# Kernel tuning notes

Measured on AMD Instinct MI355X. Metric: run time of the kernel, lower is better.

The kernel has to match this reference:

```python
import jax, jax.numpy as jnp
import numpy as np

N_NODES = 200000
N_EDGES = 240000
HIDDEN = 128
N_TYPES = 6


def setup_inputs() -> dict:
    key = jax.random.key(0)
    k1, k2, k3, k4, k5 = jax.random.split(key, 5)
    state_embedding = jax.random.normal(k1, (N_NODES, HIDDEN), dtype=jnp.float32)
    # row 0: edge type in [1, N_TYPES]; row 1: source node; row 2: target node
    etype = jax.random.randint(k2, (N_EDGES,), 1, N_TYPES + 1, dtype=jnp.int32)
    src = jax.random.randint(k3, (N_EDGES,), 0, N_NODES, dtype=jnp.int32)
    tgt = jax.random.randint(k4, (N_EDGES,), 0, N_NODES, dtype=jnp.int32)
    typed_edges = jnp.stack([etype, src, tgt], axis=0)  # [3, E]
    # stacked per-edge-type Linear(2H, H, bias=False) weights, applied as x @ W[t]
    W = jax.random.normal(k5, (N_TYPES, 2 * HIDDEN, HIDDEN), dtype=jnp.float32) / np.sqrt(2 * HIDDEN)
    return {"state_embedding": state_embedding, "typed_edges": typed_edges, "W": W}


def reference(state_embedding, typed_edges, W):
    etype, src, tgt = typed_edges[0], typed_edges[1], typed_edges[2]
    # gather source/target node states and concat -> [E, 2H]
    x = jnp.concatenate([state_embedding[src], state_embedding[tgt]], axis=1)
    n_types = W.shape[0]
    msgs = jnp.zeros((x.shape[0], W.shape[2]), dtype=x.dtype)
    # fixed small loop over edge types; masking replaces the dynamic boolean
    # filtering of the torch code (edges with type t use only W[t-1])
    for t in range(n_types):
        mask = (etype == t + 1)[:, None]
        msgs = msgs + jnp.where(mask, x @ W[t], jnp.zeros((), x.dtype))
    # scatter-add messages into target node slots, dim_size = num nodes
    return jax.ops.segment_sum(msgs, tgt, num_segments=state_embedding.shape[0])
```

## Files before the change

kernel.cpp:

```cpp
#include <hip/hip_runtime.h>

#define NTYPES 6
#define HID 128
#define E_TILE 64
#define TPB 2
#define TNBITS 19
#define TNMASK ((1 << TNBITS) - 1)
#define XST 136

typedef short short8 __attribute__((ext_vector_type(8)));
typedef float f32x4 __attribute__((ext_vector_type(4)));

static __device__ __forceinline__ ushort f2bf(float f) {
    union { float f; unsigned u; } v; v.f = f;
    unsigned r = v.u + 0x7FFFu + ((v.u >> 16) & 1u);
    return (ushort)(r >> 16);
}


__global__ void k_prep(int4* __restrict__ zp, int n4,
                       const float* __restrict__ Sf, ushort* __restrict__ Sb, int total,
                       const float* __restrict__ W, ushort* __restrict__ Wt,
                       int zb, int sb) {
    int b = blockIdx.x;
    if (b < zb) {
        int i = b * 256 + threadIdx.x;
        if (i < n4) zp[i] = make_int4(0, 0, 0, 0);
    } else if (b < zb + sb) {
        int g = ((b - zb) * 256 + threadIdx.x) * 8;
        if (g < total) {
            float4 a = *(const float4*)(Sf + g);
            float4 c = *(const float4*)(Sf + g + 4);
            ushort t[8] = { f2bf(a.x), f2bf(a.y), f2bf(a.z), f2bf(a.w),
                            f2bf(c.x), f2bf(c.y), f2bf(c.z), f2bf(c.w) };
            *(short8*)(Sb + g) = *(short8*)t;
        }
    } else {
        int t = (b - zb - sb) * 256 + threadIdx.x;
        int n  = t & 127;
        int k8 = (t >> 7) & 31;
        int ty = t >> 12;
        if (ty >= NTYPES) return;
        const float* wp = W + ((size_t)ty * 256 + (size_t)k8 * 8) * HID + n;
        ushort tmp[8];
        #pragma unroll
        for (int j = 0; j < 8; ++j) tmp[j] = f2bf(wp[(size_t)j * HID]);
        *(short8*)(Wt + ((size_t)ty * HID + n) * 256 + k8 * 8) = *(short8*)tmp;
    }
}

template <int RANK>
__global__ void k_bin(const int* __restrict__ etype, const int* __restrict__ src,
                      const int* __restrict__ tgt, int E, int CAP,
                      int* __restrict__ hdr, int* __restrict__ ncnt,
                      int2* __restrict__ sortedT2) {
    __shared__ int lcnt[NTYPES];
    __shared__ int lbase[NTYPES];
    if (threadIdx.x < NTYPES) lcnt[threadIdx.x] = 0;
    __syncthreads();
    int i = blockIdx.x * 256 + threadIdx.x;
    bool valid = (i < E);
    int sn = 0, pk = 0, t = 0, lrk = 0;
    if (valid) {
        t  = etype[i] - 1;
        int tn = tgt[i];
        sn = src[i];
        int a = 0;
        if (RANK) a = atomicAdd(&ncnt[tn], 1);
        pk  = tn | (a << TNBITS);
        lrk = atomicAdd(&lcnt[t], 1);
    }
    __syncthreads();
    if (threadIdx.x < NTYPES) {
        int c = lcnt[threadIdx.x];
        lbase[threadIdx.x] = c ? atomicAdd(&hdr[16 + threadIdx.x], c) : 0;
    }
    __syncthreads();
    if (valid) {
        int pos = lbase[t] + lrk;
        if (pos < CAP) sortedT2[(size_t)t * CAP + pos] = make_int2(sn, pk);
    }
}

__global__ void k_scan1(const int* __restrict__ ncnt, int* __restrict__ noff,
                        int* __restrict__ bsum, int N) {
    __shared__ int s[256];
    const int b = blockIdx.x, t = threadIdx.x;
    const int base = b * 1024 + t * 4;
    int v[4];
    #pragma unroll
    for (int i = 0; i < 4; ++i) v[i] = (base + i < N) ? ncnt[base + i] : 0;
    int tsum = v[0] + v[1] + v[2] + v[3];
    s[t] = tsum;
    __syncthreads();
    for (int off = 1; off < 256; off <<= 1) {
        int x = (t >= off) ? s[t - off] : 0;
        __syncthreads();
        s[t] += x;
        __syncthreads();
    }
    if (t == 255) bsum[b] = s[255];
    int run = s[t] - tsum;
    #pragma unroll
    for (int i = 0; i < 4; ++i)
        if (base + i < N) { noff[base + i] = run; run += v[i]; }
}

__global__ void k_scan2(int* __restrict__ bsum, int nb) {
    __shared__ int s[256];
    const int t = threadIdx.x;
    int v = (t < nb) ? bsum[t] : 0;
    s[t] = v;
    __syncthreads();
    for (int off = 1; off < 256; off <<= 1) {
        int x = (t >= off) ? s[t - off] : 0;
        __syncthreads();
        s[t] += x;
        __syncthreads();
    }
    if (t < nb) bsum[t] = s[t] - v;
}

template <int MODE>
__launch_bounds__(256, 4)
__global__ void k_gemm(const ushort* __restrict__ Sb, const float* __restrict__ Sf,
                       const ushort* __restrict__ Wt, const int* __restrict__ hdr,
                       const int2* __restrict__ sortedT2, int CAP,
                       const int* __restrict__ ncnt, const int* __restrict__ noff,
                       const int* __restrict__ bsum,
                       ushort* __restrict__ msgs, float* __restrict__ out) {
    __shared__ __align__(16) ushort Xs[E_TILE][XST];
    __shared__ int sN[TPB][E_TILE];
    __shared__ int tN[TPB][E_TILE];
    __shared__ int dstR[TPB][E_TILE];

    int g = blockIdx.x;
    int ty, t0 = 0, ntl = 0, cnt_t = 0;
    for (ty = 0; ty < NTYPES; ++ty) {
        int c = hdr[16 + ty];
        if (c > CAP) c = CAP;
        int nt = (c + E_TILE - 1) >> 6;
        int ng = (nt + TPB - 1) / TPB;
        if (g < ng) {
            t0 = g * TPB;
            ntl = nt - t0; if (ntl > TPB) ntl = TPB;
            cnt_t = c;
            break;
        }
        g -= ng;
    }
    if (ty == NTYPES) return;

    const int tid = threadIdx.x;
    const int w  = tid >> 6;
    const int l  = tid & 63;
    const int lr = l & 15;
    const int lg = l >> 4;

    {
        const int tt = tid >> 6, s = l;
        if (tt < ntl) {
            int gp = (t0 + tt) * E_TILE + s;
            int sn = 0, tn = 0, dr = 0;
            if (gp < cnt_t) {
                int2 v = sortedT2[(size_t)ty * CAP + gp];
                sn = v.x;
                tn = v.y & TNMASK;
                if (MODE == 2) {
                    int a = ((unsigned)v.y) >> TNBITS;
                    dr = (ncnt[tn] == 1) ? -(tn + 1)
                                         : (noff[tn] + bsum[tn >> 10] + a);
                }
            }
            sN[tt][s] = sn; tN[tt][s] = tn; dstR[tt][s] = dr;
        }
    }

    short8 wreg[16];
    {
        const ushort* wb = Wt + ((size_t)ty * HID + w * 32 + lr) * 256 + 8 * lg;
        #pragma unroll
        for (int kk = 0; kk < 8; ++kk) {
            wreg[2 * kk]     = *(const short8*)(wb + kk * 32);
            wreg[2 * kk + 1] = *(const short8*)(wb + 16 * 256 + kk * 32);
        }
    }
    __syncthreads();

    const int e = tid >> 2, q = tid & 3;

    for (int tt = 0; tt < ntl; ++tt) {
        int cnt = cnt_t - (t0 + tt) * E_TILE;
        if (cnt > E_TILE) cnt = E_TILE;

        f32x4 acc[4][2];
        #pragma unroll
        for (int mf = 0; mf < 4; ++mf)
            #pragma unroll
            for (int nf = 0; nf < 2; ++nf)
                acc[mf][nf] = (f32x4){0.f, 0.f, 0.f, 0.f};

        #pragma unroll
        for (int half = 0; half < 2; ++half) {
            {
                ushort* dp = &Xs[e][q * 32];
                if (e < cnt) {
                    const int node = half ? tN[tt][e] : sN[tt][e];
                    if (MODE == 2) {
                        const ushort* rp = Sb + (size_t)node * HID + q * 32;
                        #pragma unroll
                        for (int i = 0; i < 4; ++i)
                            *(short8*)(dp + i * 8) = *(const short8*)(rp + i * 8);
                    } else {
                        const float* rp = Sf + (size_t)node * HID + q * 32;
                        #pragma unroll
                        for (int i = 0; i < 4; ++i) {
                            float4 a = *(const float4*)(rp + i * 8);
                            float4 b = *(const float4*)(rp + i * 8 + 4);
                            ushort tmp[8] = { f2bf(a.x), f2bf(a.y), f2bf(a.z), f2bf(a.w),
                                              f2bf(b.x), f2bf(b.y), f2bf(b.z), f2bf(b.w) };
                            *(short8*)(dp + i * 8) = *(short8*)tmp;
                        }
                    }
                } else {
                    short8 z = (short8){0, 0, 0, 0, 0, 0, 0, 0};
                    #pragma unroll
                    for (int i = 0; i < 4; ++i) *(short8*)(dp + i * 8) = z;
                }
            }
            __syncthreads();

            const ushort* xb = &Xs[lr][8 * lg];
            #pragma unroll
            for (int kk = 0; kk < 4; ++kk) {
                const int k0 = kk * 32;
                const int wi = 2 * (half * 4 + kk);
                #pragma unroll
                for (int mf = 0; mf < 4; ++mf) {
                    short8 a = *(const short8*)(xb + mf * 16 * XST + k0);
                    acc[mf][0] = __builtin_amdgcn_mfma_f32_16x16x32_bf16(a, wreg[wi],     acc[mf][0], 0, 0, 0);
                    acc[mf][1] = __builtin_amdgcn_mfma_f32_16x16x32_bf16(a, wreg[wi + 1], acc[mf][1], 0, 0, 0);
                }
            }
            __syncthreads();
        }

        float (*Os)[132] = (float (*)[132])&Xs[0][0];
        #pragma unroll
        for (int h = 0; h < 2; ++h) {
            #pragma unroll
            for (int m2 = 0; m2 < 2; ++m2) {
                const int mf = h * 2 + m2;
                #pragma unroll
                for (int nf = 0; nf < 2; ++nf)
                    #pragma unroll
                    for (int r = 0; r < 4; ++r)
                        Os[m2 * 16 + lg * 4 + r][w * 32 + nf * 16 + lr] = acc[mf][nf][r];
            }
            __syncthreads();
            if (MODE == 2) {
                const int r8e = tid >> 4, cg = tid & 15;
                #pragma unroll
                for (int rr = 0; rr < 2; ++rr) {
                    int rowl = rr * 16 + r8e;
                    int row  = h * 32 + rowl;
                    if (row < cnt) {
                        int dr = dstR[tt][row];
                        float4 a = *(const float4*)&Os[rowl][cg * 8];
                        float4 b = *(const float4*)&Os[rowl][cg * 8 + 4];
                        if (dr >= 0) {
                            ushort tmp[8] = { f2bf(a.x), f2bf(a.y), f2bf(a.z), f2bf(a.w),
                                              f2bf(b.x), f2bf(b.y), f2bf(b.z), f2bf(b.w) };
                            *(short8*)(msgs + (size_t)dr * HID + cg * 8) = *(short8*)tmp;
                        } else {
                            float* op = out + (size_t)(-dr - 1) * HID + cg * 8;
                            *(float4*)op = a;
                            *(float4*)(op + 4) = b;
                        }
                    }
                }
            } else {
                const int rA = tid >> 7;
                const int c  = tid & (HID - 1);
                for (int it = 0; it < 16; ++it) {
                    int rowl = it * 2 + rA;
                    int row  = h * 32 + rowl;
                    if (row < cnt) atomicAdd(&out[(size_t)tN[tt][row] * HID + c], Os[rowl][c]);
                }
            }
            __syncthreads();
        }
    }
}

__launch_bounds__(256)
__global__ void k_scatter(const ushort* __restrict__ msgs, const int* __restrict__ noff,
                          const int* __restrict__ bsum, float* __restrict__ out,
                          int N, int Etot) {
    int node = blockIdx.x * 4 + (threadIdx.x >> 6);
    if (node >= N) return;
    int cp = threadIdx.x & 63;
    int s = noff[node] + bsum[node >> 10];
    int e = (node + 1 < N) ? (noff[node + 1] + bsum[(node + 1) >> 10]) : Etot;
    if (e - s == 1) return;
    float a0 = 0.f, a1 = 0.f;
    for (int r = s; r < e; ++r) {
        unsigned u = *(const unsigned*)(msgs + (size_t)r * HID + cp * 2);
        union { unsigned u; float f; } lo, hi;
        lo.u = u << 16; hi.u = u & 0xFFFF0000u;
        a0 += lo.f; a1 += hi.f;
    }
    *(float2*)(out + (size_t)node * HID + cp * 2) = make_float2(a0, a1);
}

extern "C" void kernel_launch(void* const* d_in, const int* in_sizes, int n_in,
                              void* d_out, int out_size, void* d_ws, size_t ws_size,
                              hipStream_t stream) {
    const float* Sf    = (const float*)d_in[0];
    const int*   edges = (const int*)d_in[1];
    const float* W     = (const float*)d_in[2];
    float* out = (float*)d_out;

    const int E = in_sizes[1] / 3;
    const int N = in_sizes[0] / HID;
    const int* etype = edges;
    const int* src   = edges + E;
    const int* tgt   = edges + 2 * E;
    int* ws = (int*)d_ws;

    const int CAP = E / 5 + 4096;

    int* ncnt = ws + 32;
    int* noff = ncnt + N;
    int* bsum = noff + N + 1;
    size_t intsEnd = (size_t)(32 + N + (N + 1) + 256) * sizeof(int);
    size_t st2Off  = (intsEnd + 255) & ~(size_t)255;
    size_t wtOff   = ((st2Off + (size_t)NTYPES * CAP * sizeof(int2)) + 255) & ~(size_t)255;
    size_t sbOff   = ((wtOff + (size_t)NTYPES * HID * 256 * 2) + 255) & ~(size_t)255;
    size_t msgsOff = ((sbOff + (size_t)N * HID * 2) + 255) & ~(size_t)255;
    size_t need2   = msgsOff + (size_t)E * HID * 2;

    const int nb1 = (N + 1023) / 1024;
    const int eb  = (E + 255) / 256;
    const int nblocks = (E + E_TILE * TPB - 1) / (E_TILE * TPB) + 2 * NTYPES;
    ushort* Wt = (ushort*)((char*)d_ws + wtOff);
    int2* sortedT2 = (int2*)((char*)d_ws + st2Off);

    if (ws_size >= need2 && nb1 <= 256 && N < (1 << TNBITS)) {
        ushort* Sb   = (ushort*)((char*)d_ws + sbOff);
        ushort* msgs = (ushort*)((char*)d_ws + msgsOff);
        const int total = N * HID;
        const int n4 = (32 + N + 3) / 4;
        const int zb = (n4 + 255) / 256;
        const int sb = (total / 8 + 255) / 256;
        const int wb = (NTYPES * HID * 32 + 255) / 256;

        k_prep<<<zb + sb + wb, 256, 0, stream>>>((int4*)ws, n4, Sf, Sb, total, W, Wt, zb, sb);
        k_bin<1><<<eb, 256, 0, stream>>>(etype, src, tgt, E, CAP, ws, ncnt, sortedT2);
        k_scan1<<<nb1, 256, 0, stream>>>(ncnt, noff, bsum, N);
        k_scan2<<<1, 256, 0, stream>>>(bsum, nb1);
        k_gemm<2><<<nblocks, 256, 0, stream>>>(Sb, Sf, Wt, ws, sortedT2, CAP,
                                               ncnt, noff, bsum, msgs, out);
        k_scatter<<<(N + 3) / 4, 256, 0, stream>>>(msgs, noff, bsum, out, N, E);
    } else {
        size_t wt0Off = ((32 * sizeof(int) + (size_t)NTYPES * CAP * sizeof(int2)) + 255) & ~(size_t)255;
        int2* sortedT0 = (int2*)((char*)d_ws + ((32 * sizeof(int) + 255) & ~(size_t)255));
        ushort* Wt0 = (ushort*)((char*)d_ws + wt0Off + 256);
        sortedT0 = (int2*)((char*)d_ws + 256);
        Wt0 = (ushort*)((char*)d_ws + 256 + (((size_t)NTYPES * CAP * sizeof(int2) + 255) & ~(size_t)255));

        k_prep<<<1 + (NTYPES * HID * 32 + 255) / 256, 256, 0, stream>>>(
            (int4*)ws, 8, nullptr, nullptr, 0, W, Wt0, 1, 0);
        hipMemsetAsync(d_out, 0, (size_t)out_size * sizeof(float), stream);
        k_bin<0><<<eb, 256, 0, stream>>>(etype, src, tgt, E, CAP, ws, nullptr, sortedT0);
        k_gemm<0><<<nblocks, 256, 0, stream>>>(nullptr, Sf, Wt0, ws, sortedT0, CAP,
                                               nullptr, nullptr, nullptr, nullptr, out);
    }
}
```

Baseline: 138.8 us.

## Stage full 256-wide edge tile once and stream weights from memory

The gather now loads the source and target rows of each 64-edge tile into one 264-wide LDS buffer in a single pass, instead of two half passes. That removes the per-half syncs and the split epilogue, which now writes all 64 rows at once. Weights are no longer held in 16 registers but loaded from global memory (L2/L1) inside the k-loop, and each block handles four tiles instead of two. This trades lower register pressure and fewer barriers for more LDS use, repeated weight loads, and fewer blocks, all of which could lower occupancy or parallelism.

```diff
diff --git a/kernel.cpp b/kernel.cpp
--- a/kernel.cpp
+++ b/kernel.cpp
@@ -3,10 +3,9 @@
 #define NTYPES 6
 #define HID 128
 #define E_TILE 64
-#define TPB 2
+#define TPB 4
 #define TNBITS 19
 #define TNMASK ((1 << TNBITS) - 1)
-#define XST 136
 
 typedef short short8 __attribute__((ext_vector_type(8)));
 typedef float f32x4 __attribute__((ext_vector_type(4)));
@@ -129,7 +128,7 @@
                        const int* __restrict__ ncnt, const int* __restrict__ noff,
                        const int* __restrict__ bsum,
                        ushort* __restrict__ msgs, float* __restrict__ out) {
-    __shared__ __align__(16) ushort Xs[E_TILE][XST];
+    __shared__ __align__(16) ushort Xs[E_TILE][264];
     __shared__ int sN[TPB][E_TILE];
     __shared__ int tN[TPB][E_TILE];
     __shared__ int dstR[TPB][E_TILE];
@@ -175,23 +174,44 @@
             sN[tt][s] = sn; tN[tt][s] = tn; dstR[tt][s] = dr;
         }
     }
-
-    short8 wreg[16];
-    {
-        const ushort* wb = Wt + ((size_t)ty * HID + w * 32 + lr) * 256 + 8 * lg;
-        #pragma unroll
-        for (int kk = 0; kk < 8; ++kk) {
-            wreg[2 * kk]     = *(const short8*)(wb + kk * 32);
-            wreg[2 * kk + 1] = *(const short8*)(wb + 16 * 256 + kk * 32);
-        }
-    }
-    __syncthreads();
-
-    const int e = tid >> 2, q = tid & 3;
+    __syncthreads();
+
+    const ushort* wb = Wt + ((size_t)ty * HID + w * 32 + lr) * 256 + 8 * lg;
 
     for (int tt = 0; tt < ntl; ++tt) {
         int cnt = cnt_t - (t0 + tt) * E_TILE;
         if (cnt > E_TILE) cnt = E_TILE;
+
+        {
+            const int e = tid >> 2, q = tid & 3;
+            ushort* dp = &Xs[e][q * 64];
+            if (e < cnt) {
+                const int node = (q & 2) ? tN[tt][e] : sN[tt][e];
+                if (MODE == 2) {
+                    const ushort* rp = Sb + (size_t)node * HID + (q & 1) * 64;
+                    short8 v[8];
+                    #pragma unroll
+                    for (int i = 0; i < 8; ++i) v[i] = *(const short8*)(rp + i * 8);
+                    #pragma unroll
+                    for (int i = 0; i < 8; ++i) *(short8*)(dp + i * 8) = v[i];
+                } else {
+                    const float* rp = Sf + (size_t)node * HID + (q & 1) * 64;
+                    #pragma unroll
+                    for (int i = 0; i < 8; ++i) {
+                        float4 a = *(const float4*)(rp + i * 8);
+                        float4 b = *(const float4*)(rp + i * 8 + 4);
+                        ushort tmp[8] = { f2bf(a.x), f2bf(a.y), f2bf(a.z), f2bf(a.w),
+                                          f2bf(b.x), f2bf(b.y), f2bf(b.z), f2bf(b.w) };
+                        *(short8*)(dp + i * 8) = *(short8*)tmp;
+                    }
+                }
+            } else {
+                short8 z = (short8){0, 0, 0, 0, 0, 0, 0, 0};
+                #pragma unroll
+                for (int i = 0; i < 8; ++i) *(short8*)(dp + i * 8) = z;
+            }
+        }
+        __syncthreads();
 
         f32x4 acc[4][2];
         #pragma unroll
@@ -200,96 +220,60 @@
             for (int nf = 0; nf < 2; ++nf)
                 acc[mf][nf] = (f32x4){0.f, 0.f, 0.f, 0.f};
 
+        const ushort* xb = &Xs[lr][8 * lg];
         #pragma unroll
-        for (int half = 0; half < 2; ++half) {
-            {
-                ushort* dp = &Xs[e][q * 32];
-                if (e < cnt) {
-                    const int node = half ? tN[tt][e] : sN[tt][e];
-                    if (MODE == 2) {
-                        const ushort* rp = Sb + (size_t)node * HID + q * 32;
-                        #pragma unroll
-                        for (int i = 0; i < 4; ++i)
-                            *(short8*)(dp + i * 8) = *(const short8*)(rp + i * 8);
-                    } else {
-                        const float* rp = Sf + (size_t)node * HID + q * 32;
-                        #pragma unroll
-                        for (int i = 0; i < 4; ++i) {
-                            float4 a = *(const float4*)(rp + i * 8);
-                            float4 b = *(const float4*)(rp + i * 8 + 4);
-                            ushort tmp[8] = { f2bf(a.x), f2bf(a.y), f2bf(a.z), f2bf(a.w),
-                                              f2bf(b.x), f2bf(b.y), f2bf(b.z), f2bf(b.w) };
-                            *(short8*)(dp + i * 8) = *(short8*)tmp;
-                        }
-                    }
-                } else {
-                    short8 z = (short8){0, 0, 0, 0, 0, 0, 0, 0};
-                    #pragma unroll
-                    for (int i = 0; i < 4; ++i) *(short8*)(dp + i * 8) = z;
-                }
-            }
-            __syncthreads();
-
-            const ushort* xb = &Xs[lr][8 * lg];
+        for (int kk = 0; kk < 8; ++kk) {
+            const int k0 = kk * 32;
+            short8 b0 = *(const short8*)(wb + k0);
+            short8 b1 = *(const short8*)(wb + 16 * 256 + k0);
             #pragma unroll
-            for (int kk = 0; kk < 4; ++kk) {
-                const int k0 = kk * 32;
-                const int wi = 2 * (half * 4 + kk);
-                #pragma unroll
-                for (int mf = 0; mf < 4; ++mf) {
-                    short8 a = *(const short8*)(xb + mf * 16 * XST + k0);
-                    acc[mf][0] = __builtin_amdgcn_mfma_f32_16x16x32_bf16(a, wreg[wi],     acc[mf][0], 0, 0, 0);
-                    acc[mf][1] = __builtin_amdgcn_mfma_f32_16x16x32_bf16(a, wreg[wi + 1], acc[mf][1], 0, 0, 0);
-                }
-            }
-            __syncthreads();
-        }
+            for (int mf = 0; mf < 4; ++mf) {
+                short8 a = *(const short8*)(xb + mf * 16 * 264 + k0);
+                acc[mf][0] = __builtin_amdgcn_mfma_f32_16x16x32_bf16(a, b0, acc[mf][0], 0, 0, 0);
+                acc[mf][1] = __builtin_amdgcn_mfma_f32_16x16x32_bf16(a, b1, acc[mf][1], 0, 0, 0);
+            }
+        }
+        __syncthreads();
 
         float (*Os)[132] = (float (*)[132])&Xs[0][0];
         #pragma unroll
-        for (int h = 0; h < 2; ++h) {
+        for (int mf = 0; mf < 4; ++mf)
             #pragma unroll
-            for (int m2 = 0; m2 < 2; ++m2) {
-                const int mf = h * 2 + m2;
+            for (int nf = 0; nf < 2; ++nf)
                 #pragma unroll
-                for (int nf = 0; nf < 2; ++nf)
-                    #pragma unroll
-                    for (int r = 0; r < 4; ++r)
-                        Os[m2 * 16 + lg * 4 + r][w * 32 + nf * 16 + lr] = acc[mf][nf][r];
-            }
-            __syncthreads();
-            if (MODE == 2) {
-                const int r8e = tid >> 4, cg = tid & 15;
-                #pragma unroll
-                for (int rr = 0; rr < 2; ++rr) {
-                    int rowl = rr * 16 + r8e;
-                    int row  = h * 32 + rowl;
-                    if (row < cnt) {
-                        int dr = dstR[tt][row];
-                        float4 a = *(const float4*)&Os[rowl][cg * 8];
-                        float4 b = *(const float4*)&Os[rowl][cg * 8 + 4];
-                        if (dr >= 0) {
-                            ushort tmp[8] = { f2bf(a.x), f2bf(a.y), f2bf(a.z), f2bf(a.w),
-                                              f2bf(b.x), f2bf(b.y), f2bf(b.z), f2bf(b.w) };
-                            *(short8*)(msgs + (size_t)dr * HID + cg * 8) = *(short8*)tmp;
-                        } else {
-                            float* op = out + (size_t)(-dr - 1) * HID + cg * 8;
-                            *(float4*)op = a;
-                            *(float4*)(op + 4) = b;
-                        }
+                for (int r = 0; r < 4; ++r)
+                    Os[mf * 16 + lg * 4 + r][w * 32 + nf * 16 + lr] = acc[mf][nf][r];
+        __syncthreads();
+
+        if (MODE == 2) {
+            const int r8e = tid >> 4, cg = tid & 15;
+            #pragma unroll
+            for (int rr = 0; rr < 4; ++rr) {
+                int row = rr * 16 + r8e;
+                if (row < cnt) {
+                    int dr = dstR[tt][row];
+                    float4 a = *(const float4*)&Os[row][cg * 8];
+                    float4 b = *(const float4*)&Os[row][cg * 8 + 4];
+                    if (dr >= 0) {
+                        ushort tmp[8] = { f2bf(a.x), f2bf(a.y), f2bf(a.z), f2bf(a.w),
+                                          f2bf(b.x), f2bf(b.y), f2bf(b.z), f2bf(b.w) };
+                        *(short8*)(msgs + (size_t)dr * HID + cg * 8) = *(short8*)tmp;
+                    } else {
+                        float* op = out + (size_t)(-dr - 1) * HID + cg * 8;
+                        *(float4*)op = a;
+                        *(float4*)(op + 4) = b;
                     }
                 }
-            } else {
-                const int rA = tid >> 7;
-                const int c  = tid & (HID - 1);
-                for (int it = 0; it < 16; ++it) {
-                    int rowl = it * 2 + rA;
-                    int row  = h * 32 + rowl;
-                    if (row < cnt) atomicAdd(&out[(size_t)tN[tt][row] * HID + c], Os[rowl][c]);
-                }
-            }
-            __syncthreads();
-        }
+            }
+        } else {
+            const int rA = tid >> 7;
+            const int c  = tid & (HID - 1);
+            for (int it = 0; it < E_TILE / 2; ++it) {
+                int ee = it * 2 + rA;
+                if (ee < cnt) atomicAdd(&out[(size_t)tN[tt][ee] * HID + c], Os[ee][c]);
+            }
+        }
+        __syncthreads();
     }
 }
 
@@ -363,11 +347,9 @@
                                                ncnt, noff, bsum, msgs, out);
         k_scatter<<<(N + 3) / 4, 256, 0, stream>>>(msgs, noff, bsum, out, N, E);
     } else {
-        size_t wt0Off = ((32 * sizeof(int) + (size_t)NTYPES * CAP * sizeof(int2)) + 255) & ~(size_t)255;
-        int2* sortedT0 = (int2*)((char*)d_ws + ((32 * sizeof(int) + 255) & ~(size_t)255));
-        ushort* Wt0 = (ushort*)((char*)d_ws + wt0Off + 256);
-        sortedT0 = (int2*)((char*)d_ws + 256);
-        Wt0 = (ushort*)((char*)d_ws + 256 + (((size_t)NTYPES * CAP * sizeof(int2) + 255) & ~(size_t)255));
+        int2* sortedT0 = (int2*)((char*)d_ws + 256);
+        ushort* Wt0 = (ushort*)((char*)d_ws + 256 +
+                      (((size_t)NTYPES * CAP * sizeof(int2) + 255) & ~(size_t)255));
 
         k_prep<<<1 + (NTYPES * HID * 32 + 255) / 256, 256, 0, stream>>>(
             (int4*)ws, 8, nullptr, nullptr, 0, W, Wt0, 1, 0);
```

After: 132.0 us, median of 2. -5.0%, faster.
